# Kernel tuning notes

Hardware: AMD Instinct MI355X
Metric: run time of the kernel (lower is better)

Reference implementation:

```python
import jax, jax.numpy as jnp
import numpy as np
from jax import lax

NUM_VARS = 16384
NUM_CHECKS = 8192
BATCH = 32
MAX_ITER = 15
H_DENSITY = 0.001  # ~8 ones per column, LDPC-like Tanner graph


def setup_inputs() -> dict:
    key = jax.random.key(0)
    k_h, k_s, k_l = jax.random.split(key, 3)
    # Sparse binary parity-check matrix represented densely (same math).
    parity_matrix = (jax.random.uniform(k_h, (NUM_CHECKS, NUM_VARS)) < H_DENSITY).astype(jnp.float32)
    syndrome = jax.random.randint(k_s, (BATCH, NUM_CHECKS), 0, 2).astype(jnp.float32)
    channel_llrs = jax.random.normal(k_l, (BATCH, NUM_VARS), dtype=jnp.float32)
    w_vc = jnp.ones((1,), dtype=jnp.float32)
    w_cv = jnp.ones((1,), dtype=jnp.float32)
    damping = jnp.float32(0.5)
    return {
        "syndrome": syndrome,
        "parity_matrix": parity_matrix,
        "channel_llrs": channel_llrs,
        "w_vc": w_vc,
        "w_cv": w_cv,
        "damping": damping,
    }


def reference(syndrome, parity_matrix, channel_llrs, w_vc, w_cv, damping):
    # syndrome: (B, C); parity_matrix H: (C, V); channel_llrs: (B, V)
    s_sign = 1.0 - 2.0 * syndrome  # (B, C)

    def body(v_beliefs, _):
        # v -> c: sparse.mm(H, v^T)^T == v @ H^T  -> (B, C)
        v_to_c = w_vc * (v_beliefs @ parity_matrix.T)
        c_msg = s_sign * jnp.tanh(v_to_c * 0.5)  # (B, C)
        # c -> v: sparse.mm(H^T, c^T)^T == c @ H  -> (B, V)
        c_to_v = w_cv * (c_msg @ parity_matrix)
        v_new = damping * v_beliefs + (1.0 - damping) * (channel_llrs + c_to_v)
        return v_new, None

    v_beliefs, _ = lax.scan(body, channel_llrs, None, length=MAX_ITER)
    return jax.nn.sigmoid(-v_beliefs)  # (B, V) bit-flip probabilities
```

## Files before the change

### kernel.cpp

```cpp
#include <hip/hip_runtime.h>


#define C_NUM 8192
#define V_NUM 16384
#define B_NUM 32
#define RW 64
#define CW 32

#define NBLK 256
#define NTHR 1024
#define NTH (NBLK * NTHR)

typedef unsigned short u16;
typedef unsigned int u32;
typedef unsigned long long u64;

#define ZERO_WORDS ((C_NUM * 4 + V_NUM * 4 + C_NUM * RW * 2 + V_NUM * CW * 2) / 4)
#define NBAR 31
#define BAR_STRIDE 64

__device__ __forceinline__ float agent_ldf(const float* p) {
    return __hip_atomic_load(p, __ATOMIC_RELAXED, __HIP_MEMORY_SCOPE_AGENT);
}
__device__ __forceinline__ void agent_stf(float* p, float v) {
    __hip_atomic_store(p, v, __ATOMIC_RELAXED, __HIP_MEMORY_SCOPE_AGENT);
}
__device__ __forceinline__ u64 agent_ld64(const u64* p) {
    return __hip_atomic_load(p, __ATOMIC_RELAXED, __HIP_MEMORY_SCOPE_AGENT);
}
__device__ __forceinline__ int agent_ldi(const int* p) {
    return __hip_atomic_load(p, __ATOMIC_RELAXED, __HIP_MEMORY_SCOPE_AGENT);
}
__device__ __forceinline__ void agent_st32(u32* p, u32 v) {
    __hip_atomic_store(p, v, __ATOMIC_RELAXED, __HIP_MEMORY_SCOPE_AGENT);
}
__device__ __forceinline__ void agent_st16(u16* p, u16 v) {
    __hip_atomic_store(p, v, __ATOMIC_RELAXED, __HIP_MEMORY_SCOPE_AGENT);
}

__device__ __forceinline__ void grid_barrier(u32* bars, int id) {
    __syncthreads();
    if (threadIdx.x == 0) {
        u32* base = bars + id * 8 * BAR_STRIDE;
        asm volatile("s_waitcnt vmcnt(0) lgkmcnt(0)" ::: "memory");
        __hip_atomic_fetch_add(base + (blockIdx.x & 7) * BAR_STRIDE, 1u,
                               __ATOMIC_RELAXED, __HIP_MEMORY_SCOPE_AGENT);
        u32 sum;
        do {
            sum = 0;
#pragma unroll
            for (int g = 0; g < 8; ++g)
                sum += __hip_atomic_load(base + g * BAR_STRIDE,
                                         __ATOMIC_RELAXED, __HIP_MEMORY_SCOPE_AGENT);
            if (sum < (u32)NBLK) __builtin_amdgcn_s_sleep(4);
        } while (sum < (u32)NBLK);
        asm volatile("" ::: "memory");
    }
    __syncthreads();
}

__device__ __forceinline__ float fast_tanh_half(float x) {
    float ax = fabsf(x);
    float e = __expf(-ax);
    return copysignf((1.0f - e) / (1.0f + e), x);
}

__global__ __launch_bounds__(NTHR, 1)
void bp_fused(const float* __restrict__ H,
              const float* __restrict__ synd,
              const float* __restrict__ llr,
              const float* __restrict__ w_vc_p,
              const float* __restrict__ w_cv_p,
              const float* __restrict__ damp_p,
              int* __restrict__ row_cnt, int* __restrict__ col_cnt,
              u16* __restrict__ row_idx, u16* __restrict__ col_idx,
              float* __restrict__ bel, float* __restrict__ cms,
              u32* __restrict__ bars,
              float* __restrict__ out) {
    const int tid = blockIdx.x * NTHR + threadIdx.x;

    {
        u32* zp = (u32*)row_cnt;
        for (int t = tid; t < ZERO_WORDS; t += NTH) agent_st32(&zp[t], 0u);
    }
    float llr_r[2], bel_r[2];
#pragma unroll
    for (int r = 0; r < 2; ++r) {
        int i = tid + r * NTH;
        int b = i & 31, v = i >> 5;
        float x = llr[b * V_NUM + v];
        llr_r[r] = x; bel_r[r] = x;
        agent_stf(&bel[i], x);
    }
    float ss_r;
    {
        int b = tid & 31, c = tid >> 5;
        ss_r = 1.0f - 2.0f * synd[b * C_NUM + c];
    }
    grid_barrier(bars, 0);

    {
        const int total4 = C_NUM * V_NUM / 4;
        const float4* Hv = (const float4*)H;
        for (int t = tid; t < total4; t += 2 * NTH) {
            float4 h0 = Hv[t];
            float4 h1 = Hv[t + NTH];
#pragma unroll
            for (int half = 0; half < 2; ++half) {
                float4 hv = half ? h1 : h0;
                int base = (half ? (t + NTH) : t) * 4;
                float vals[4] = {hv.x, hv.y, hv.z, hv.w};
#pragma unroll
                for (int k = 0; k < 4; ++k) {
                    if (vals[k] != 0.0f) {
                        int ee = base + k;
                        int c = ee >> 14;
                        int v = ee & (V_NUM - 1);
                        int rs = atomicAdd(&row_cnt[c], 1);
                        if (rs < RW) agent_st16(&row_idx[c * RW + rs], (u16)v);
                        int cs = atomicAdd(&col_cnt[v], 1);
                        if (cs < CW) agent_st16(&col_idx[v * CW + cs], (u16)c);
                    }
                }
            }
        }
    }
    grid_barrier(bars, 1);

    int nrow_r;
    {
        int n = agent_ldi(&row_cnt[tid >> 5]);
        nrow_r = n > RW ? RW : n;
    }
    int ncol_r[2];
#pragma unroll
    for (int r = 0; r < 2; ++r) {
        int n = agent_ldi(&col_cnt[(tid + r * NTH) >> 5]);
        ncol_r[r] = n > CW ? CW : n;
    }
    const float wvc = w_vc_p[0];
    const float wcv = w_cv_p[0];
    const float d   = damp_p[0];

    int barid = 2;
    for (int it = 0; it < 15; ++it) {
        {
            int b = tid & 31, c = tid >> 5;
            int n = nrow_r;
            const u64* q4 = (const u64*)(row_idx + c * RW);
            float sum = 0.0f;
            int k4 = (n + 3) >> 2;
            for (int p = 0; p < k4; ++p) {
                u64 q = agent_ld64(&q4[p]);
                int j = 4 * p;
                int i0 = (int)(q & 0xFFFFu);
                int i1 = (int)((q >> 16) & 0xFFFFu);
                int i2 = (int)((q >> 32) & 0xFFFFu);
                int i3 = (int)(q >> 48);
                float s0 = agent_ldf(&bel[i0 * B_NUM + b]);
                float s1 = agent_ldf(&bel[i1 * B_NUM + b]);
                float s2 = agent_ldf(&bel[i2 * B_NUM + b]);
                float s3 = agent_ldf(&bel[i3 * B_NUM + b]);
                sum += s0;
                sum += (j + 1 < n) ? s1 : 0.0f;
                sum += (j + 2 < n) ? s2 : 0.0f;
                sum += (j + 3 < n) ? s3 : 0.0f;
            }
            agent_stf(&cms[tid], ss_r * fast_tanh_half(wvc * sum));
        }
        grid_barrier(bars, barid++);

        bool last = (it == 14);
#pragma unroll
        for (int r = 0; r < 2; ++r) {
            int i = tid + r * NTH;
            int b = i & 31, v = i >> 5;
            int n = ncol_r[r];
            const u64* q4 = (const u64*)(col_idx + v * CW);
            float sum = 0.0f;
            int k4 = (n + 3) >> 2;
            for (int p = 0; p < k4; ++p) {
                u64 q = agent_ld64(&q4[p]);
                int j = 4 * p;
                int i0 = (int)(q & 0xFFFFu);
                int i1 = (int)((q >> 16) & 0xFFFFu);
                int i2 = (int)((q >> 32) & 0xFFFFu);
                int i3 = (int)(q >> 48);
                float s0 = agent_ldf(&cms[i0 * B_NUM + b]);
                float s1 = agent_ldf(&cms[i1 * B_NUM + b]);
                float s2 = agent_ldf(&cms[i2 * B_NUM + b]);
                float s3 = agent_ldf(&cms[i3 * B_NUM + b]);
                sum += s0;
                sum += (j + 1 < n) ? s1 : 0.0f;
                sum += (j + 2 < n) ? s2 : 0.0f;
                sum += (j + 3 < n) ? s3 : 0.0f;
            }
            float nb = d * bel_r[r] + (1.0f - d) * (llr_r[r] + wcv * sum);
            bel_r[r] = nb;
            if (!last) {
                agent_stf(&bel[i], nb);
            } else {
                out[b * V_NUM + v] = 1.0f / (1.0f + __expf(nb));
            }
        }
        if (!last) grid_barrier(bars, barid++);
    }
}

extern "C" void kernel_launch(void* const* d_in, const int* in_sizes, int n_in,
                              void* d_out, int out_size, void* d_ws, size_t ws_size,
                              hipStream_t stream) {
    const float* synd = (const float*)d_in[0];
    const float* H    = (const float*)d_in[1];
    const float* llr  = (const float*)d_in[2];
    const float* w_vc = (const float*)d_in[3];
    const float* w_cv = (const float*)d_in[4];
    const float* damp = (const float*)d_in[5];
    float* out = (float*)d_out;

    char* ws = (char*)d_ws;
    size_t off = 0;
    int* row_cnt = (int*)(ws + off); off += (size_t)C_NUM * 4;
    int* col_cnt = (int*)(ws + off); off += (size_t)V_NUM * 4;
    u16* row_idx = (u16*)(ws + off); off += (size_t)C_NUM * RW * 2;
    u16* col_idx = (u16*)(ws + off); off += (size_t)V_NUM * CW * 2;
    float* bel = (float*)(ws + off); off += (size_t)V_NUM * B_NUM * 4;
    float* cms = (float*)(ws + off); off += (size_t)C_NUM * B_NUM * 4;
    u32* bars  = (u32*)(ws + off); off += (size_t)NBAR * 8 * BAR_STRIDE * 4;

    hipMemsetAsync(bars, 0, (size_t)NBAR * 8 * BAR_STRIDE * 4, stream);

    void* args[] = {
        (void*)&H, (void*)&synd, (void*)&llr,
        (void*)&w_vc, (void*)&w_cv, (void*)&damp,
        (void*)&row_cnt, (void*)&col_cnt, (void*)&row_idx, (void*)&col_idx,
        (void*)&bel, (void*)&cms, (void*)&bars, (void*)&out
    };
    hipLaunchCooperativeKernel((const void*)bp_fused,
                               dim3(NBLK), dim3(NTHR), args, 0, stream);
}
```

Baseline: 988.0 us.

## Compact H nonzeros into LDS per wave, overlapping scan with zeroing barrier

The dense H scan now runs before the first grid barrier. Each wave compacts nonzero edge indices into a shared-memory list using ballot and popcount, and only after the barrier does it issue the atomic row and column inserts from that list. This lets the 512 MB read of H overlap with the workspace zeroing and packs the atomics densely across lanes, where before they ran in divergent branches. The risk is that a wave holding more than WCAP=256 nonzeros silently drops edges. The expected count is about 134 per wave, so overflow is unlikely but not guarded.

```diff
diff --git a/kernel.cpp b/kernel.cpp
--- a/kernel.cpp
+++ b/kernel.cpp
@@ -10,6 +10,8 @@
 #define NBLK 256
 #define NTHR 1024
 #define NTH (NBLK * NTHR)
+
+#define WCAP 256
 
 typedef unsigned short u16;
 typedef unsigned int u32;
@@ -78,6 +80,10 @@
               u32* __restrict__ bars,
               float* __restrict__ out) {
     const int tid = blockIdx.x * NTHR + threadIdx.x;
+    const int lane = threadIdx.x & 63;
+
+    __shared__ u32 lds_edges[(NTHR / 64) * WCAP];
+    u32* const wl = lds_edges + (threadIdx.x >> 6) * WCAP;
 
     {
         u32* zp = (u32*)row_cnt;
@@ -97,32 +103,46 @@
         int b = tid & 31, c = tid >> 5;
         ss_r = 1.0f - 2.0f * synd[b * C_NUM + c];
     }
-    grid_barrier(bars, 0);
-
-    {
-        const int total4 = C_NUM * V_NUM / 4;
+
+    int wave_cnt;
+    {
         const float4* Hv = (const float4*)H;
-        for (int t = tid; t < total4; t += 2 * NTH) {
+        const u64 ltmask = (1ull << lane) - 1ull;
+        int wb = 0;
+#pragma unroll 2
+        for (int itn = 0; itn < 64; ++itn) {
+            int t = tid + itn * (2 * NTH);
             float4 h0 = Hv[t];
             float4 h1 = Hv[t + NTH];
-#pragma unroll
-            for (int half = 0; half < 2; ++half) {
-                float4 hv = half ? h1 : h0;
-                int base = (half ? (t + NTH) : t) * 4;
-                float vals[4] = {hv.x, hv.y, hv.z, hv.w};
-#pragma unroll
-                for (int k = 0; k < 4; ++k) {
-                    if (vals[k] != 0.0f) {
-                        int ee = base + k;
-                        int c = ee >> 14;
-                        int v = ee & (V_NUM - 1);
-                        int rs = atomicAdd(&row_cnt[c], 1);
-                        if (rs < RW) agent_st16(&row_idx[c * RW + rs], (u16)v);
-                        int cs = atomicAdd(&col_cnt[v], 1);
-                        if (cs < CW) agent_st16(&col_idx[v * CW + cs], (u16)c);
+            float vals[8] = {h0.x, h0.y, h0.z, h0.w, h1.x, h1.y, h1.z, h1.w};
+#pragma unroll
+            for (int k = 0; k < 8; ++k) {
+                bool nz = vals[k] != 0.0f;
+                u64 b = __ballot(nz);
+                if (b) {
+                    if (nz) {
+                        int ee = (k < 4) ? (t * 4 + k)
+                                         : ((t + NTH) * 4 + (k - 4));
+                        int off = wb + (int)__popcll(b & ltmask);
+                        if (off < WCAP) wl[off] = (u32)ee;
                     }
+                    wb += (int)__popcll(b);
                 }
             }
+        }
+        wave_cnt = wb < WCAP ? wb : WCAP;
+    }
+    grid_barrier(bars, 0);
+
+    {
+        for (int e = lane; e < wave_cnt; e += 64) {
+            u32 ee = wl[e];
+            int c = (int)(ee >> 14);
+            int v = (int)(ee & (V_NUM - 1));
+            int rs = atomicAdd(&row_cnt[c], 1);
+            if (rs < RW) agent_st16(&row_idx[c * RW + rs], (u16)v);
+            int cs = atomicAdd(&col_cnt[v], 1);
+            if (cs < CW) agent_st16(&col_idx[v * CW + cs], (u16)c);
         }
     }
     grid_barrier(bars, 1);
```

Result: no change. 980.7 us (-0.7%).
